# Kernel optimization log

Hardware: AMD Instinct MI355X
Metric: run time of the kernel (lower is better)

## Reference

```python
import jax, jax.numpy as jnp
import numpy as np

N = 50000        # nodes
E = 1600000      # edges (avg degree 32)
D = 64           # emb_dim
H = 2            # heads
NEG_SLOPE = 0.2
BOND_VOCAB = 5   # vocab per bond feature (3 categorical features)


def setup_inputs() -> dict:
    key = jax.random.key(0)
    ks = jax.random.split(key, 8)
    x = jax.random.normal(ks[0], (N, D), jnp.float32)
    edge_index = jax.random.randint(ks[1], (2, E), 0, N)
    edge_attr = jax.random.randint(ks[2], (E, 3), 0, BOND_VOCAB)
    W = jax.random.normal(ks[3], (D, H * D), jnp.float32) / np.float32(np.sqrt(D))
    b_W = jnp.zeros((H * D,), jnp.float32)
    att = jax.random.normal(ks[4], (1, H, 2 * D), jnp.float32) * 0.1
    bias = jnp.zeros((D,), jnp.float32)
    bond_emb = jax.random.normal(ks[5], (3, BOND_VOCAB, H * D), jnp.float32) * 0.1
    return dict(x=x, edge_index=edge_index, edge_attr=edge_attr,
                W=W, b_W=b_W, att=att, bias=bias, bond_emb=bond_emb)


def reference(x, edge_index, edge_attr, W, b_W, att, bias, bond_emb):
    row, col = edge_index[0], edge_index[1]  # src (x_j), dst (x_i / aggregation target)
    # BondEncoder: sum of per-feature categorical embeddings -> [E, H*D]
    e = (bond_emb[0][edge_attr[:, 0]]
         + bond_emb[1][edge_attr[:, 1]]
         + bond_emb[2][edge_attr[:, 2]])
    h = x @ W + b_W                                   # [N, H*D]
    x_j = h[row].reshape(-1, H, D) + e.reshape(-1, H, D)   # message source + edge emb
    x_i = h[col].reshape(-1, H, D)                         # message target
    # attention logits: [E, H]
    alpha = (jnp.concatenate([x_i, x_j], axis=-1) * att).sum(-1)
    alpha = jnp.where(alpha >= 0, alpha, NEG_SLOPE * alpha)  # leaky_relu
    # segment softmax over edge_index[0] (source node), PyG semantics
    m = jax.ops.segment_max(alpha, row, num_segments=N)      # [N, H]
    m = jnp.where(jnp.isfinite(m), m, 0.0)                   # empty segments -> 0
    ea = jnp.exp(alpha - m[row])
    s = jax.ops.segment_sum(ea, row, num_segments=N)
    alpha = ea / (s[row] + 1e-16)
    # weighted messages, scatter-add to destination nodes
    msg = x_j * alpha[:, :, None]                            # [E, H, D]
    aggr = jax.ops.segment_sum(msg, col, num_segments=N)     # [N, H, D]
    # update: mean over heads + bias
    return aggr.mean(axis=1) + bias
```

## Files before the change

kernel.cpp:

```cpp
#include <hip/hip_runtime.h>
#include <hip/hip_bf16.h>
#include <math.h>

#define NEG_SLOPE 0.2f
#define CHUNK 2048
#define NPB2 128
#define SCAP 5120

__device__ __forceinline__ unsigned f2bf(float f) {
  unsigned u = __float_as_uint(f);
  return (u + 0x7fffu + ((u >> 16) & 1u)) >> 16;
}

__global__ __launch_bounds__(256) void k1_gemm(
    const float* __restrict__ x, const float* __restrict__ W,
    const float* __restrict__ bW, const float* __restrict__ att,
    unsigned int* __restrict__ hb, float* __restrict__ ai,
    float* __restrict__ aj, int Nn) {
  int t = threadIdx.x;
  int lane = t & 63;
  int wid = blockIdx.x * (blockDim.x >> 6) + (t >> 6);
  int nwaves = gridDim.x * (blockDim.x >> 6);

  float Wr0[64], Wr1[64];
#pragma unroll
  for (int k = 0; k < 64; ++k) {
    Wr0[k] = W[k * 128 + lane];
    Wr1[k] = W[k * 128 + 64 + lane];
  }
  float bs0 = bW[lane], bs1 = bW[64 + lane];
  float ati0 = att[lane];
  float atj0 = att[64 + lane];
  float ati1 = att[128 + lane];
  float atj1 = att[192 + lane];

  for (int row = wid; row < Nn; row += nwaves) {
    int r = __builtin_amdgcn_readfirstlane(row);
    const float* __restrict__ xr = x + (size_t)r * 64;
    float a0a = 0.f, a0b = 0.f, a1a = 0.f, a1b = 0.f;
#pragma unroll
    for (int k = 0; k < 64; k += 2) {
      float xk0 = xr[k], xk1 = xr[k + 1];
      a0a = fmaf(xk0, Wr0[k], a0a);
      a1a = fmaf(xk0, Wr1[k], a1a);
      a0b = fmaf(xk1, Wr0[k + 1], a0b);
      a1b = fmaf(xk1, Wr1[k + 1], a1b);
    }
    float h0 = a0a + a0b + bs0;
    float h1 = a1a + a1b + bs1;
    hb[(size_t)r * 64 + lane] = f2bf(h0) | (f2bf(h1) << 16);

    float ti0 = ati0 * h0, tj0 = atj0 * h0;
    float ti1 = ati1 * h1, tj1 = atj1 * h1;
    ti0 += __shfl_xor(ti0, 32, 64);
    tj0 += __shfl_xor(tj0, 32, 64);
    ti1 += __shfl_xor(ti1, 32, 64);
    tj1 += __shfl_xor(tj1, 32, 64);
    float mi = (lane < 32) ? ti0 : ti1;
    float mj = (lane < 32) ? tj0 : tj1;
#pragma unroll
    for (int off = 16; off > 0; off >>= 1) {
      mi += __shfl_xor(mi, off, 64);
      mj += __shfl_xor(mj, off, 64);
    }
    if ((lane & 31) == 0) {
      ai[r * 2 + (lane >> 5)] = mi;
      aj[r * 2 + (lane >> 5)] = mj;
    }
  }
}

__global__ __launch_bounds__(256) void k_bin(
    const int* __restrict__ ei, const int* __restrict__ eattr,
    unsigned int* __restrict__ rec, int* __restrict__ cnt_tbl,
    int* __restrict__ base_tbl, unsigned int* __restrict__ rec_src,
    int* __restrict__ cnt_tbl2, int* __restrict__ base_tbl2, int Ee, int NCB) {
  __shared__ unsigned sbuf[CHUNK];
  __shared__ unsigned sbuf2[CHUNK];
  __shared__ int hist[512], cur[512], hist2[512], cur2[512];
  __shared__ int ssc[256];
  int t = threadIdx.x;
  for (int i = t; i < NCB; i += 256) { hist[i] = 0; hist2[i] = 0; }
  __syncthreads();
  int start = blockIdx.x * CHUNK;
  int end = min(start + CHUNK, Ee);
  int cnt = end - start;
  int cbv[CHUNK / 256], cb2v[CHUNK / 256];
  unsigned pkv[CHUNK / 256], pk2v[CHUNK / 256];
  int nk = 0;
  for (int e = start + t; e < end; e += 256, ++nk) {
    int dst = __builtin_nontemporal_load(&ei[Ee + e]);
    int src = __builtin_nontemporal_load(&ei[e]);
    int a0 = __builtin_nontemporal_load(&eattr[e * 3]);
    int a1 = __builtin_nontemporal_load(&eattr[e * 3 + 1]);
    int a2 = __builtin_nontemporal_load(&eattr[e * 3 + 2]);
    unsigned c012 = (unsigned)(a0 + 5 * a1 + 25 * a2);
    cbv[nk] = dst >> 7;
    pkv[nk] = (unsigned)src | (c012 << 16) | ((unsigned)(dst & 127) << 23);
    cb2v[nk] = src >> 7;
    pk2v[nk] = (unsigned)dst | ((unsigned)(src & 127) << 17) | (c012 << 24);
    atomicAdd(&hist[dst >> 7], 1);
    atomicAdd(&hist2[src >> 7], 1);
  }
  __syncthreads();
  {
    int per = (NCB + 255) / 256;
    int loc[4];
    int lsum = 0;
#pragma unroll 2
    for (int j = 0; j < per; ++j) {
      int idx = t * per + j;
      int v = (idx < NCB) ? hist[idx] : 0;
      loc[j] = lsum;
      lsum += v;
    }
    ssc[t] = lsum;
    __syncthreads();
#pragma unroll
    for (int o = 1; o < 256; o <<= 1) {
      int xv = (t >= o) ? ssc[t - o] : 0;
      __syncthreads();
      ssc[t] += xv;
      __syncthreads();
    }
    int excl = ssc[t] - lsum;
#pragma unroll 2
    for (int j = 0; j < per; ++j) {
      int idx = t * per + j;
      if (idx < NCB) cur[idx] = excl + loc[j];
    }
    __syncthreads();
    lsum = 0;
#pragma unroll 2
    for (int j = 0; j < per; ++j) {
      int idx = t * per + j;
      int v = (idx < NCB) ? hist2[idx] : 0;
      loc[j] = lsum;
      lsum += v;
    }
    ssc[t] = lsum;
    __syncthreads();
#pragma unroll
    for (int o = 1; o < 256; o <<= 1) {
      int xv = (t >= o) ? ssc[t - o] : 0;
      __syncthreads();
      ssc[t] += xv;
      __syncthreads();
    }
    excl = ssc[t] - lsum;
#pragma unroll 2
    for (int j = 0; j < per; ++j) {
      int idx = t * per + j;
      if (idx < NCB) cur2[idx] = excl + loc[j];
    }
  }
  __syncthreads();
  for (int i = t; i < NCB; i += 256) {
    cnt_tbl[blockIdx.x * NCB + i] = hist[i];
    base_tbl[blockIdx.x * NCB + i] = cur[i];
    cnt_tbl2[blockIdx.x * NCB + i] = hist2[i];
    base_tbl2[blockIdx.x * NCB + i] = cur2[i];
  }
  __syncthreads();
  for (int k = 0; k < nk; ++k) {
    int pos = atomicAdd(&cur[cbv[k]], 1);
    sbuf[pos] = pkv[k];
    int pos2 = atomicAdd(&cur2[cb2v[k]], 1);
    sbuf2[pos2] = pk2v[k];
  }
  __syncthreads();
  for (int i = t; i < cnt; i += 256) {
    __builtin_nontemporal_store(sbuf[i], &rec[start + i]);
    __builtin_nontemporal_store(sbuf2[i], &rec_src[start + i]);
  }
}

__global__ __launch_bounds__(256) void k_segoff_ab(
    const int* __restrict__ cnt_tbl, int* __restrict__ segdst,
    int* __restrict__ btot, const int* __restrict__ cnt_tbl2,
    int* __restrict__ segdst2, int* __restrict__ btot2, int NCB, int NBLK) {
  __shared__ int s[256];
  int t = threadIdx.x;
  int bid = blockIdx.x;
  const int* __restrict__ ct = (bid < NCB) ? cnt_tbl : cnt_tbl2;
  int* __restrict__ sd = (bid < NCB) ? segdst : segdst2;
  int* __restrict__ bt = (bid < NCB) ? btot : btot2;
  int cb = (bid < NCB) ? bid : bid - NCB;
  int per = (NBLK + 255) / 256;
  int loc[8];
  int sum = 0;
  for (int j = 0; j < per; ++j) {
    int blk = t * per + j;
    int v = (blk < NBLK) ? ct[blk * NCB + cb] : 0;
    loc[j] = sum;
    sum += v;
  }
  s[t] = sum;
  __syncthreads();
#pragma unroll
  for (int o = 1; o < 256; o <<= 1) {
    int xv = (t >= o) ? s[t - o] : 0;
    __syncthreads();
    s[t] += xv;
    __syncthreads();
  }
  int excl = s[t] - sum;
  for (int j = 0; j < per; ++j) {
    int blk = t * per + j;
    if (blk < NBLK) sd[cb * NBLK + blk] = excl + loc[j];
  }
  if (t == 255) bt[cb] = s[255];
}

__global__ __launch_bounds__(512) void k_segoff_b(
    const int* __restrict__ btot, int* __restrict__ coarse_base, int NCB, int Ee) {
  __shared__ int s[512];
  int t = threadIdx.x;
  int v = (t < NCB) ? btot[t] : 0;
  s[t] = v;
  __syncthreads();
#pragma unroll
  for (int o = 1; o < 512; o <<= 1) {
    int xv = (t >= o) ? s[t - o] : 0;
    __syncthreads();
    s[t] += xv;
    __syncthreads();
  }
  if (t < NCB) coarse_base[t] = s[t] - v;
  if (t == 0) coarse_base[NCB] = Ee;
}

__global__ __launch_bounds__(256) void k_mid(
    const unsigned int* __restrict__ rec, const int* __restrict__ cnt_tbl,
    const int* __restrict__ base_tbl, const int* __restrict__ segdst,
    const int* __restrict__ coarse_base,
    const unsigned int* __restrict__ rec_src, const int* __restrict__ cnt_tbl2,
    const int* __restrict__ base_tbl2, const int* __restrict__ segdst2,
    const int* __restrict__ btot2,
    const float2* __restrict__ ai2, const float2* __restrict__ aj2,
    const float* __restrict__ att, const float* __restrict__ bemb,
    float* __restrict__ rden, unsigned int* __restrict__ eix2,
    float2* __restrict__ alpha2, int* __restrict__ off,
    int Nn, int NCB, int NBLK, int Ee) {
  __shared__ unsigned ubuf[SCAP];
  __shared__ unsigned ubuf2[SCAP];
  __shared__ int hist[NPB2], basex[NPB2], curx[NPB2];
  __shared__ float tbl[30];
  __shared__ float2 nodev[NPB2];
  __shared__ float sdl[NPB2 * 2];
  int t = threadIdx.x;
  if (t < 30) {
    int f = t / 10, rem = t % 10, c = rem >> 1, hh = rem & 1;
    float sacc = 0.f;
    for (int d = 0; d < 64; ++d)
      sacc += att[hh * 128 + 64 + d] * bemb[(f * 5 + c) * 128 + hh * 64 + d];
    tbl[t] = sacc;
  }

  if (blockIdx.x < NCB) {
    int cb = blockIdx.x;
    int node0 = cb << 7;
    if (t < NPB2 && node0 + t < Nn) nodev[t] = aj2[node0 + t];
    sdl[t] = 0.f;
    int total = btot2[cb];
    __syncthreads();
    bool fits = (total <= SCAP);

#define SACC_BODY(U, AIV)                                                      \
    {                                                                          \
      int sl = ((U) >> 17) & 127;                                              \
      int c012 = ((U) >> 24) & 127;                                            \
      int a0 = c012 % 5, a1 = (c012 / 5) % 5, a2 = c012 / 25;                  \
      float2 ajv = nodev[sl];                                                  \
      float lg0 = AIV.x + ajv.x + tbl[a0 * 2] + tbl[10 + a1 * 2] +             \
                  tbl[20 + a2 * 2];                                            \
      float lg1 = AIV.y + ajv.y + tbl[a0 * 2 + 1] + tbl[10 + a1 * 2 + 1] +     \
                  tbl[20 + a2 * 2 + 1];                                        \
      lg0 = lg0 >= 0.f ? lg0 : NEG_SLOPE * lg0;                                \
      lg1 = lg1 >= 0.f ? lg1 : NEG_SLOPE * lg1;                                \
      atomicAdd(&sdl[sl * 2], __expf(lg0));                                    \
      atomicAdd(&sdl[sl * 2 + 1], __expf(lg1));                                \
    }

    if (fits) {
      for (int blk = t; blk < NBLK; blk += 256) {
        int len = cnt_tbl2[blk * NCB + cb];
        if (!len) continue;
        int sp = blk * CHUNK + base_tbl2[blk * NCB + cb];
        int dp = segdst2[cb * NBLK + blk];
        for (int j = 0; j < len; ++j) ubuf[dp + j] = rec_src[sp + j];
      }
      __syncthreads();
      int i = t;
      for (; i + 7 * 256 < total; i += 8 * 256) {
        unsigned u[8];
        float2 aiv[8];
#pragma unroll
        for (int k = 0; k < 8; ++k) u[k] = ubuf[i + k * 256];
#pragma unroll
        for (int k = 0; k < 8; ++k) aiv[k] = ai2[u[k] & 0x1FFFF];
#pragma unroll
        for (int k = 0; k < 8; ++k) SACC_BODY(u[k], aiv[k])
      }
      for (; i < total; i += 256) {
        unsigned u = ubuf[i];
        float2 aiv = ai2[u & 0x1FFFF];
        SACC_BODY(u, aiv)
      }
    } else {
      for (int blk = t; blk < NBLK; blk += 256) {
        int len = cnt_tbl2[blk * NCB + cb];
        int sp = blk * CHUNK + base_tbl2[blk * NCB + cb];
        for (int j = 0; j < len; ++j) {
          unsigned u = rec_src[sp + j];
          float2 aiv = ai2[u & 0x1FFFF];
          SACC_BODY(u, aiv)
        }
      }
    }
#undef SACC_BODY
    __syncthreads();
    if (node0 + (t >> 1) < Nn)
      rden[(size_t)node0 * 2 + t] = 1.0f / (sdl[t] + 1e-16f);

  } else {
    int cb = blockIdx.x - NCB;
    int node0 = cb << 7;
    if (t < NPB2) {
      hist[t] = 0;
      if (node0 + t < Nn) nodev[t] = ai2[node0 + t];
    }
    int gbase = coarse_base[cb];
    int total = coarse_base[cb + 1] - gbase;
    __syncthreads();
    bool fits = (total <= SCAP);

    if (fits) {
      for (int blk = t; blk < NBLK; blk += 256) {
        int len = cnt_tbl[blk * NCB + cb];
        if (!len) continue;
        int sp = blk * CHUNK + base_tbl[blk * NCB + cb];
        int dp = segdst[cb * NBLK + blk];
        for (int j = 0; j < len; ++j) ubuf[dp + j] = rec[sp + j];
      }
      __syncthreads();
      for (int i = t; i < total; i += 256)
        atomicAdd(&hist[(ubuf[i] >> 23) & 127], 1);
      __syncthreads();
      if (t == 0) {
        int s = 0;
        for (int i = 0; i < NPB2; ++i) { basex[i] = s; s += hist[i]; }
      }
      __syncthreads();
      if (t < NPB2) {
        curx[t] = basex[t];
        if (node0 + t < Nn) off[node0 + t] = gbase + basex[t];
      }
      if (cb == 0 && t == 0) off[Nn] = Ee;
      __syncthreads();
      for (int i = t; i < total; i += 256) {
        unsigned u = ubuf[i];
        int pos = atomicAdd(&curx[(u >> 23) & 127], 1);
        ubuf2[pos] = u;
      }
      __syncthreads();

#define OUT_BODY(I, U, AJV)                                                    \
      {                                                                        \
        int src = (U) & 0xFFFF;                                                \
        int c012 = ((U) >> 16) & 127;                                          \
        int dl = ((U) >> 23) & 127;                                            \
        int a0 = c012 % 5, a1 = (c012 / 5) % 5, a2 = c012 / 25;                \
        float2 aiv = nodev[dl];                                                \
        float lg0 = aiv.x + AJV.x + tbl[a0 * 2] + tbl[10 + a1 * 2] +           \
                    tbl[20 + a2 * 2];                                          \
        float lg1 = aiv.y + AJV.y + tbl[a0 * 2 + 1] + tbl[10 + a1 * 2 + 1] +   \
                    tbl[20 + a2 * 2 + 1];                                      \
        lg0 = lg0 >= 0.f ? lg0 : NEG_SLOPE * lg0;                              \
        lg1 = lg1 >= 0.f ? lg1 : NEG_SLOPE * lg1;                              \
        eix2[gbase + (I)] = (unsigned)src | ((unsigned)a0 << 16) |             \
                            ((unsigned)a1 << 19) | ((unsigned)a2 << 22);       \
        alpha2[gbase + (I)] = make_float2(__expf(lg0), __expf(lg1));           \
      }

      int i = t;
      for (; i + 7 * 256 < total; i += 8 * 256) {
        unsigned u[8];
        float2 ajv[8];
#pragma unroll
        for (int k = 0; k < 8; ++k) u[k] = ubuf2[i + k * 256];
#pragma unroll
        for (int k = 0; k < 8; ++k) ajv[k] = aj2[u[k] & 0xFFFF];
#pragma unroll
        for (int k = 0; k < 8; ++k) OUT_BODY(i + k * 256, u[k], ajv[k])
      }
      for (; i < total; i += 256) {
        unsigned u = ubuf2[i];
        float2 ajv = aj2[u & 0xFFFF];
        OUT_BODY(i, u, ajv)
      }
#undef OUT_BODY
    } else {
      for (int blk = t; blk < NBLK; blk += 256) {
        int len = cnt_tbl[blk * NCB + cb];
        int sp = blk * CHUNK + base_tbl[blk * NCB + cb];
        for (int j = 0; j < len; ++j)
          atomicAdd(&hist[(rec[sp + j] >> 23) & 127], 1);
      }
      __syncthreads();
      if (t == 0) {
        int s = 0;
        for (int i = 0; i < NPB2; ++i) { basex[i] = s; s += hist[i]; }
      }
      __syncthreads();
      if (t < NPB2) {
        curx[t] = basex[t];
        if (node0 + t < Nn) off[node0 + t] = gbase + basex[t];
      }
      if (cb == 0 && t == 0) off[Nn] = Ee;
      __syncthreads();
      for (int blk = t; blk < NBLK; blk += 256) {
        int len = cnt_tbl[blk * NCB + cb];
        int sp = blk * CHUNK + base_tbl[blk * NCB + cb];
        for (int j = 0; j < len; ++j) {
          unsigned u = rec[sp + j];
          int src = u & 0xFFFF;
          int c012 = (u >> 16) & 127;
          int dl = (u >> 23) & 127;
          int a0 = c012 % 5, a1 = (c012 / 5) % 5, a2 = c012 / 25;
          float2 aiv = nodev[dl];
          float2 ajv = aj2[src];
          float lg0 = aiv.x + ajv.x + tbl[a0 * 2] + tbl[10 + a1 * 2] +
                      tbl[20 + a2 * 2];
          float lg1 = aiv.y + ajv.y + tbl[a0 * 2 + 1] + tbl[10 + a1 * 2 + 1] +
                      tbl[20 + a2 * 2 + 1];
          lg0 = lg0 >= 0.f ? lg0 : NEG_SLOPE * lg0;
          lg1 = lg1 >= 0.f ? lg1 : NEG_SLOPE * lg1;
          int pos = gbase + atomicAdd(&curx[dl], 1);
          eix2[pos] = (unsigned)src | ((unsigned)a0 << 16) |
                      ((unsigned)a1 << 19) | ((unsigned)a2 << 22);
          alpha2[pos] = make_float2(__expf(lg0), __expf(lg1));
        }
      }
    }
  }
}

__global__ __launch_bounds__(256) void k_norm(
    const unsigned int* __restrict__ eix, float2* __restrict__ alpha2,
    const float2* __restrict__ rden2, int Ee) {
  int g = blockIdx.x * 256 + threadIdx.x;
  int e = g * 4;
  if (e + 4 <= Ee) {
    uint4 u = *reinterpret_cast<const uint4*>(&eix[e]);
    float2 rd0 = rden2[u.x & 0xFFFFu];
    float2 rd1 = rden2[u.y & 0xFFFFu];
    float2 rd2 = rden2[u.z & 0xFFFFu];
    float2 rd3 = rden2[u.w & 0xFFFFu];
    float4 a01 = *reinterpret_cast<float4*>(&alpha2[e]);
    float4 a23 = *reinterpret_cast<float4*>(&alpha2[e + 2]);
    a01.x *= rd0.x; a01.y *= rd0.y; a01.z *= rd1.x; a01.w *= rd1.y;
    a23.x *= rd2.x; a23.y *= rd2.y; a23.z *= rd3.x; a23.w *= rd3.y;
    *reinterpret_cast<float4*>(&alpha2[e]) = a01;
    *reinterpret_cast<float4*>(&alpha2[e + 2]) = a23;
  } else {
    for (; e < Ee; ++e) {
      unsigned u = eix[e];
      float2 rd = rden2[u & 0xFFFFu];
      float2 a = alpha2[e];
      alpha2[e] = make_float2(a.x * rd.x, a.y * rd.y);
    }
  }
}

__global__ __launch_bounds__(256) void k_gather(
    const unsigned int* __restrict__ eix, const float2* __restrict__ alpha2,
    const int* __restrict__ off, const unsigned int* __restrict__ hb,
    const float* __restrict__ bemb, const float* __restrict__ bias,
    float* __restrict__ out, int Nn) {
  __shared__ float bembs[15 * 128];
  __shared__ float wsm[4][32];
  int t = threadIdx.x;
  for (int i = t; i < 15 * 128; i += 256) bembs[i] = bemb[i];
  __syncthreads();
  int wave = t >> 6, lane = t & 63;
  int n = blockIdx.x * 4 + wave;
  if (n >= Nn) return;
  int p0 = __builtin_amdgcn_readfirstlane(off[n]);
  int p1 = __builtin_amdgcn_readfirstlane(off[n + 1]);
  int myf = lane / 5;
  int myc = lane % 5;
  bool active = lane < 15;
  int myshift = 16 + 3 * myf;
  int mycEff = active ? myc : 8;
  float w0 = 0.f, w1 = 0.f;
  float acc0 = 0.f, acc1 = 0.f;

#define EDGE_BODY(U, HV, AL)                                                   \
  {                                                                            \
    acc0 = fmaf((AL).x, __uint_as_float((HV) << 16), acc0);                    \
    acc1 = fmaf((AL).y, __uint_as_float((HV) & 0xffff0000u), acc1);            \
    int sel = (int)(((U) >> myshift) & 7u);                                    \
    float m = (sel == mycEff) ? 1.0f : 0.0f;                                   \
    w0 = fmaf(m, (AL).x, w0);                                                  \
    w1 = fmaf(m, (AL).y, w1);                                                  \
  }

  int p = p0;
  for (; p + 8 <= p1; p += 8) {
    unsigned u[8], hv[8];
    float2 al[8];
#pragma unroll
    for (int k = 0; k < 8; ++k) u[k] = eix[p + k];
#pragma unroll
    for (int k = 0; k < 8; ++k) al[k] = alpha2[p + k];
#pragma unroll
    for (int k = 0; k < 8; ++k) {
      const unsigned* __restrict__ hrow = hb + ((size_t)(u[k] & 0xFFFFu) << 6);
      hv[k] = hrow[lane];
    }
#pragma unroll
    for (int k = 0; k < 8; ++k) EDGE_BODY(u[k], hv[k], al[k])
  }
  for (; p < p1; ++p) {
    unsigned ue = eix[p];
    float2 ale = alpha2[p];
    const unsigned* __restrict__ hrow = hb + ((size_t)(ue & 0xFFFFu) << 6);
    unsigned hve = hrow[lane];
    EDGE_BODY(ue, hve, ale)
  }
#undef EDGE_BODY

  if (active) {
    wsm[wave][lane * 2] = w0;
    wsm[wave][lane * 2 + 1] = w1;
  }
#pragma unroll
  for (int k = 0; k < 15; ++k) {
    acc0 += wsm[wave][k * 2] * bembs[k * 128 + lane];
    acc1 += wsm[wave][k * 2 + 1] * bembs[k * 128 + 64 + lane];
  }
  out[(size_t)n * 64 + lane] = 0.5f * (acc0 + acc1) + bias[lane];
}

extern "C" void kernel_launch(void* const* d_in, const int* in_sizes, int n_in,
                              void* d_out, int out_size, void* d_ws, size_t ws_size,
                              hipStream_t stream) {
  const float* x    = (const float*)d_in[0];
  const int*   ei   = (const int*)d_in[1];
  const int*   eatt = (const int*)d_in[2];
  const float* W    = (const float*)d_in[3];
  const float* bW   = (const float*)d_in[4];
  const float* att  = (const float*)d_in[5];
  const float* bias = (const float*)d_in[6];
  const float* bemb = (const float*)d_in[7];
  int Nn = in_sizes[0] / 64;
  int Ee = in_sizes[1] / 2;
  int NCB = (Nn + NPB2 - 1) / NPB2;
  int NBLK = (Ee + CHUNK - 1) / CHUNK;

  char* ws = (char*)d_ws;
  ws = (char*)(((uintptr_t)ws + 15) & ~(uintptr_t)15);
  float* aj = (float*)ws;                 ws += (size_t)Nn * 2 * 4;
  float* rden = (float*)ws;               ws += (size_t)Nn * 2 * 4;
  float* ai = (float*)ws;                 ws += (size_t)Nn * 2 * 4;
  unsigned int* hb = (unsigned int*)ws;   ws += (size_t)Nn * 64 * 4;
  unsigned int* rec = (unsigned int*)ws;  ws += (size_t)NBLK * CHUNK * 4;
  unsigned int* rec_src = (unsigned int*)ws; ws += (size_t)NBLK * CHUNK * 4;
  unsigned int* eix2 = (unsigned int*)ws; ws += (size_t)Ee * 4;
  float2* alpha2 = (float2*)ws;           ws += (size_t)Ee * 8;
  int* off = (int*)ws;                    ws += (size_t)(Nn + 1) * 4;
  int* cnt_tbl = (int*)ws;                ws += (size_t)NBLK * NCB * 4;
  int* base_tbl = (int*)ws;               ws += (size_t)NBLK * NCB * 4;
  int* cnt_tbl2 = (int*)ws;               ws += (size_t)NBLK * NCB * 4;
  int* base_tbl2 = (int*)ws;              ws += (size_t)NBLK * NCB * 4;
  int* segdst = (int*)ws;                 ws += (size_t)NCB * NBLK * 4;
  int* segdst2 = (int*)ws;                ws += (size_t)NCB * NBLK * 4;
  int* coarse_base = (int*)ws;            ws += (size_t)(NCB + 1) * 4;
  int* btot = (int*)ws;                   ws += (size_t)NCB * 4;
  int* btot2 = (int*)ws;                  ws += (size_t)NCB * 4;

  k1_gemm<<<1024, 256, 0, stream>>>(x, W, bW, att, hb, ai, aj, Nn);
  k_bin<<<NBLK, 256, 0, stream>>>(ei, eatt, rec, cnt_tbl, base_tbl, rec_src,
                                  cnt_tbl2, base_tbl2, Ee, NCB);
  k_segoff_ab<<<2 * NCB, 256, 0, stream>>>(cnt_tbl, segdst, btot, cnt_tbl2,
                                           segdst2, btot2, NCB, NBLK);
  k_segoff_b<<<1, 512, 0, stream>>>(btot, coarse_base, NCB, Ee);
  k_mid<<<2 * NCB, 256, 0, stream>>>(rec, cnt_tbl, base_tbl, segdst,
                                     coarse_base, rec_src, cnt_tbl2, base_tbl2,
                                     segdst2, btot2, (const float2*)ai,
                                     (const float2*)aj, att, bemb, rden, eix2,
                                     alpha2, off, Nn, NCB, NBLK, Ee);
  k_norm<<<(Ee / 4 + 255) / 256, 256, 0, stream>>>(eix2, alpha2,
                                                   (const float2*)rden, Ee);
  k_gather<<<(Nn + 3) / 4, 256, 0, stream>>>(eix2, alpha2, off, hb, bemb, bias,
                                             (float*)d_out, Nn);
}
```

Baseline: 276.8 us.

## Defer logit/exp computation to k_norm using packed aj+rden per-node float4

Stops computing attention logits and exponentials in the dst-sort pass of k_mid, which now just stores the destination node's ai value per edge. The logit, leaky-relu, exp and reciprocal-denominator multiply move into k_norm. That kernel fetches one packed float4 per source node holding aj and rden, replacing the separate random gather of aj in k_mid and of rden in k_norm. The bond-attention table is computed once in k_segoff_b and stored globally. This removes one random gather per edge but puts more ALU work into k_norm and changes its vector loads into scalar float2 accesses.

Result: no change. 274.4 us (-0.9%).

```diff
diff --git a/kernel.cpp b/kernel.cpp
--- a/kernel.cpp
+++ b/kernel.cpp
@@ -16,7 +16,7 @@
     const float* __restrict__ x, const float* __restrict__ W,
     const float* __restrict__ bW, const float* __restrict__ att,
     unsigned int* __restrict__ hb, float* __restrict__ ai,
-    float* __restrict__ aj, int Nn) {
+    float* __restrict__ ajrd, int Nn) {
   int t = threadIdx.x;
   int lane = t & 63;
   int wid = blockIdx.x * (blockDim.x >> 6) + (t >> 6);
@@ -65,7 +65,7 @@
     }
     if ((lane & 31) == 0) {
       ai[r * 2 + (lane >> 5)] = mi;
-      aj[r * 2 + (lane >> 5)] = mj;
+      ajrd[(size_t)r * 4 + (lane >> 5)] = mj;
     }
   }
 }
@@ -213,9 +213,18 @@
 }
 
 __global__ __launch_bounds__(512) void k_segoff_b(
-    const int* __restrict__ btot, int* __restrict__ coarse_base, int NCB, int Ee) {
+    const int* __restrict__ btot, int* __restrict__ coarse_base,
+    const float* __restrict__ att, const float* __restrict__ bemb,
+    float* __restrict__ tblg, int NCB, int Ee) {
   __shared__ int s[512];
   int t = threadIdx.x;
+  if (t < 30) {
+    int f = t / 10, rem = t % 10, c = rem >> 1, hh = rem & 1;
+    float sacc = 0.f;
+    for (int d = 0; d < 64; ++d)
+      sacc += att[hh * 128 + 64 + d] * bemb[(f * 5 + c) * 128 + hh * 64 + d];
+    tblg[t] = sacc;
+  }
   int v = (t < NCB) ? btot[t] : 0;
   s[t] = v;
   __syncthreads();
@@ -237,11 +246,10 @@
     const unsigned int* __restrict__ rec_src, const int* __restrict__ cnt_tbl2,
     const int* __restrict__ base_tbl2, const int* __restrict__ segdst2,
     const int* __restrict__ btot2,
-    const float2* __restrict__ ai2, const float2* __restrict__ aj2,
+    const float2* __restrict__ ai2, float* __restrict__ ajrd,
     const float* __restrict__ att, const float* __restrict__ bemb,
-    float* __restrict__ rden, unsigned int* __restrict__ eix2,
-    float2* __restrict__ alpha2, int* __restrict__ off,
-    int Nn, int NCB, int NBLK, int Ee) {
+    unsigned int* __restrict__ eix2, float2* __restrict__ alpha2,
+    int* __restrict__ off, int Nn, int NCB, int NBLK, int Ee) {
   __shared__ unsigned ubuf[SCAP];
   __shared__ unsigned ubuf2[SCAP];
   __shared__ int hist[NPB2], basex[NPB2], curx[NPB2];
@@ -260,7 +268,8 @@
   if (blockIdx.x < NCB) {
     int cb = blockIdx.x;
     int node0 = cb << 7;
-    if (t < NPB2 && node0 + t < Nn) nodev[t] = aj2[node0 + t];
+    if (t < NPB2 && node0 + t < Nn)
+      nodev[t] = *(const float2*)(ajrd + (size_t)(node0 + t) * 4);
     sdl[t] = 0.f;
     int total = btot2[cb];
     __syncthreads();
@@ -320,8 +329,11 @@
     }
 #undef SACC_BODY
     __syncthreads();
-    if (node0 + (t >> 1) < Nn)
-      rden[(size_t)node0 * 2 + t] = 1.0f / (sdl[t] + 1e-16f);
+    {
+      int node = node0 + (t >> 1);
+      if (node < Nn)
+        ajrd[(size_t)node * 4 + 2 + (t & 1)] = 1.0f / (sdl[t] + 1e-16f);
+    }
 
   } else {
     int cb = blockIdx.x - NCB;
@@ -364,42 +376,16 @@
         ubuf2[pos] = u;
       }
       __syncthreads();
-
-#define OUT_BODY(I, U, AJV)                                                    \
-      {                                                                        \
-        int src = (U) & 0xFFFF;                                                \
-        int c012 = ((U) >> 16) & 127;                                          \
-        int dl = ((U) >> 23) & 127;                                            \
-        int a0 = c012 % 5, a1 = (c012 / 5) % 5, a2 = c012 / 25;                \
-        float2 aiv = nodev[dl];                                                \
-        float lg0 = aiv.x + AJV.x + tbl[a0 * 2] + tbl[10 + a1 * 2] +           \
-                    tbl[20 + a2 * 2];                                          \
-        float lg1 = aiv.y + AJV.y + tbl[a0 * 2 + 1] + tbl[10 + a1 * 2 + 1] +   \
-                    tbl[20 + a2 * 2 + 1];                                      \
-        lg0 = lg0 >= 0.f ? lg0 : NEG_SLOPE * lg0;                              \
-        lg1 = lg1 >= 0.f ? lg1 : NEG_SLOPE * lg1;                              \
-        eix2[gbase + (I)] = (unsigned)src | ((unsigned)a0 << 16) |             \
-                            ((unsigned)a1 << 19) | ((unsigned)a2 << 22);       \
-        alpha2[gbase + (I)] = make_float2(__expf(lg0), __expf(lg1));           \
-      }
-
-      int i = t;
-      for (; i + 7 * 256 < total; i += 8 * 256) {
-        unsigned u[8];
-        float2 ajv[8];
-#pragma unroll
-        for (int k = 0; k < 8; ++k) u[k] = ubuf2[i + k * 256];
-#pragma unroll
-        for (int k = 0; k < 8; ++k) ajv[k] = aj2[u[k] & 0xFFFF];
-#pragma unroll
-        for (int k = 0; k < 8; ++k) OUT_BODY(i + k * 256, u[k], ajv[k])
-      }
-      for (; i < total; i += 256) {
+      for (int i = t; i < total; i += 256) {
         unsigned u = ubuf2[i];
-        float2 ajv = aj2[u & 0xFFFF];
-        OUT_BODY(i, u, ajv)
-      }
-#undef OUT_BODY
+        int src = u & 0xFFFF;
+        int c012 = (u >> 16) & 127;
+        int dl = (u >> 23) & 127;
+        int a0 = c012 % 5, a1 = (c012 / 5) % 5, a2 = c012 / 25;
+        eix2[gbase + i] = (unsigned)src | ((unsigned)a0 << 16) |
+                          ((unsigned)a1 << 19) | ((unsigned)a2 << 22);
+        alpha2[gbase + i] = nodev[dl];
+      }
     } else {
       for (int blk = t; blk < NBLK; blk += 256) {
         int len = cnt_tbl[blk * NCB + cb];
@@ -428,18 +414,10 @@
           int c012 = (u >> 16) & 127;
           int dl = (u >> 23) & 127;
           int a0 = c012 % 5, a1 = (c012 / 5) % 5, a2 = c012 / 25;
-          float2 aiv = nodev[dl];
-          float2 ajv = aj2[src];
-          float lg0 = aiv.x + ajv.x + tbl[a0 * 2] + tbl[10 + a1 * 2] +
-                      tbl[20 + a2 * 2];
-          float lg1 = aiv.y + ajv.y + tbl[a0 * 2 + 1] + tbl[10 + a1 * 2 + 1] +
-                      tbl[20 + a2 * 2 + 1];
-          lg0 = lg0 >= 0.f ? lg0 : NEG_SLOPE * lg0;
-          lg1 = lg1 >= 0.f ? lg1 : NEG_SLOPE * lg1;
           int pos = gbase + atomicAdd(&curx[dl], 1);
           eix2[pos] = (unsigned)src | ((unsigned)a0 << 16) |
                       ((unsigned)a1 << 19) | ((unsigned)a2 << 22);
-          alpha2[pos] = make_float2(__expf(lg0), __expf(lg1));
+          alpha2[pos] = nodev[dl];
         }
       }
     }
@@ -448,29 +426,52 @@
 
 __global__ __launch_bounds__(256) void k_norm(
     const unsigned int* __restrict__ eix, float2* __restrict__ alpha2,
-    const float2* __restrict__ rden2, int Ee) {
-  int g = blockIdx.x * 256 + threadIdx.x;
+    const float4* __restrict__ ajrd4, const float* __restrict__ tblg, int Ee) {
+  __shared__ float tbl[30];
+  int t = threadIdx.x;
+  if (t < 30) tbl[t] = tblg[t];
+  __syncthreads();
+
+#define NORM_BODY(U, A, F, OUT)                                                \
+  {                                                                            \
+    int a0 = ((U) >> 16) & 7, a1 = ((U) >> 19) & 7, a2 = ((U) >> 22) & 7;      \
+    float lg0 = (A).x + (F).x + tbl[a0 * 2] + tbl[10 + a1 * 2] +               \
+                tbl[20 + a2 * 2];                                              \
+    float lg1 = (A).y + (F).y + tbl[a0 * 2 + 1] + tbl[10 + a1 * 2 + 1] +       \
+                tbl[20 + a2 * 2 + 1];                                          \
+    lg0 = lg0 >= 0.f ? lg0 : NEG_SLOPE * lg0;                                  \
+    lg1 = lg1 >= 0.f ? lg1 : NEG_SLOPE * lg1;                                  \
+    OUT = make_float2(__expf(lg0) * (F).z, __expf(lg1) * (F).w);               \
+  }
+
+  int g = blockIdx.x * 256 + t;
   int e = g * 4;
   if (e + 4 <= Ee) {
     uint4 u = *reinterpret_cast<const uint4*>(&eix[e]);
-    float2 rd0 = rden2[u.x & 0xFFFFu];
-    float2 rd1 = rden2[u.y & 0xFFFFu];
-    float2 rd2 = rden2[u.z & 0xFFFFu];
-    float2 rd3 = rden2[u.w & 0xFFFFu];
-    float4 a01 = *reinterpret_cast<float4*>(&alpha2[e]);
-    float4 a23 = *reinterpret_cast<float4*>(&alpha2[e + 2]);
-    a01.x *= rd0.x; a01.y *= rd0.y; a01.z *= rd1.x; a01.w *= rd1.y;
-    a23.x *= rd2.x; a23.y *= rd2.y; a23.z *= rd3.x; a23.w *= rd3.y;
-    *reinterpret_cast<float4*>(&alpha2[e]) = a01;
-    *reinterpret_cast<float4*>(&alpha2[e + 2]) = a23;
+    float4 f0 = ajrd4[u.x & 0xFFFFu];
+    float4 f1 = ajrd4[u.y & 0xFFFFu];
+    float4 f2 = ajrd4[u.z & 0xFFFFu];
+    float4 f3 = ajrd4[u.w & 0xFFFFu];
+    float2 a0v = alpha2[e], a1v = alpha2[e + 1];
+    float2 a2v = alpha2[e + 2], a3v = alpha2[e + 3];
+    float2 o0, o1, o2, o3;
+    NORM_BODY(u.x, a0v, f0, o0)
+    NORM_BODY(u.y, a1v, f1, o1)
+    NORM_BODY(u.z, a2v, f2, o2)
+    NORM_BODY(u.w, a3v, f3, o3)
+    alpha2[e] = o0; alpha2[e + 1] = o1;
+    alpha2[e + 2] = o2; alpha2[e + 3] = o3;
   } else {
     for (; e < Ee; ++e) {
       unsigned u = eix[e];
-      float2 rd = rden2[u & 0xFFFFu];
+      float4 f = ajrd4[u & 0xFFFFu];
       float2 a = alpha2[e];
-      alpha2[e] = make_float2(a.x * rd.x, a.y * rd.y);
-    }
-  }
+      float2 o;
+      NORM_BODY(u, a, f, o)
+      alpha2[e] = o;
+    }
+  }
+#undef NORM_BODY
 }
 
 __global__ __launch_bounds__(256) void k_gather(
@@ -561,9 +562,9 @@
 
   char* ws = (char*)d_ws;
   ws = (char*)(((uintptr_t)ws + 15) & ~(uintptr_t)15);
-  float* aj = (float*)ws;                 ws += (size_t)Nn * 2 * 4;
-  float* rden = (float*)ws;               ws += (size_t)Nn * 2 * 4;
+  float* ajrd = (float*)ws;               ws += (size_t)Nn * 4 * 4;
   float* ai = (float*)ws;                 ws += (size_t)Nn * 2 * 4;
+  float* tblg = (float*)ws;               ws += 32 * 4;
   unsigned int* hb = (unsigned int*)ws;   ws += (size_t)Nn * 64 * 4;
   unsigned int* rec = (unsigned int*)ws;  ws += (size_t)NBLK * CHUNK * 4;
   unsigned int* rec_src = (unsigned int*)ws; ws += (size_t)NBLK * CHUNK * 4;
@@ -580,19 +581,19 @@
   int* btot = (int*)ws;                   ws += (size_t)NCB * 4;
   int* btot2 = (int*)ws;                  ws += (size_t)NCB * 4;
 
-  k1_gemm<<<1024, 256, 0, stream>>>(x, W, bW, att, hb, ai, aj, Nn);
+  k1_gemm<<<1024, 256, 0, stream>>>(x, W, bW, att, hb, ai, ajrd, Nn);
   k_bin<<<NBLK, 256, 0, stream>>>(ei, eatt, rec, cnt_tbl, base_tbl, rec_src,
                                   cnt_tbl2, base_tbl2, Ee, NCB);
   k_segoff_ab<<<2 * NCB, 256, 0, stream>>>(cnt_tbl, segdst, btot, cnt_tbl2,
                                            segdst2, btot2, NCB, NBLK);
-  k_segoff_b<<<1, 512, 0, stream>>>(btot, coarse_base, NCB, Ee);
+  k_segoff_b<<<1, 512, 0, stream>>>(btot, coarse_base, att, bemb, tblg, NCB, Ee);
   k_mid<<<2 * NCB, 256, 0, stream>>>(rec, cnt_tbl, base_tbl, segdst,
                                      coarse_base, rec_src, cnt_tbl2, base_tbl2,
-                                     segdst2, btot2, (const float2*)ai,
-                                     (const float2*)aj, att, bemb, rden, eix2,
-                                     alpha2, off, Nn, NCB, NBLK, Ee);
+                                     segdst2, btot2, (const float2*)ai, ajrd,
+                                     att, bemb, eix2, alpha2, off,
+                                     Nn, NCB, NBLK, Ee);
   k_norm<<<(Ee / 4 + 255) / 256, 256, 0, stream>>>(eix2, alpha2,
-                                                   (const float2*)rden, Ee);
+                                                   (const float4*)ajrd, tblg, Ee);
   k_gather<<<(Nn + 3) / 4, 256, 0, stream>>>(eix2, alpha2, off, hb, bemb, bias,
                                              (float*)d_out, Nn);
 }
```
